# Optimization experiments

Measured on AMD Instinct MI355X. Metric: run time of the kernel, lower is better.

The kernel has to match this reference:

```python
import jax, jax.numpy as jnp
import numpy as np

N, E, G, B, L = 24576, 98304, 512, 512, 1000
F_IN, H1, C1, C2, HID = 5, 2, 64, 128, 256


def setup_inputs() -> dict:
    key = jax.random.key(0)
    ks = jax.random.split(key, 20)
    rn = lambda k, s: jax.random.normal(k, s, jnp.float32) * 0.1
    return {
        "x": jax.random.normal(ks[0], (N, F_IN), jnp.float32),
        "edge_index": jax.random.randint(ks[1], (2, E), 0, N),
        "batch": jnp.sort(jax.random.randint(ks[2], (N,), 0, G)),
        "protein_seq": jax.random.randint(ks[3], (B, L), 0, 22),
        "W1": rn(ks[4], (F_IN, H1 * C1)), "att_src1": rn(ks[5], (H1, C1)), "att_dst1": rn(ks[6], (H1, C1)), "b1": jnp.zeros((H1 * C1,), jnp.float32),
        "W2": rn(ks[7], (H1 * C1, C2)), "att_src2": rn(ks[8], (1, C2)), "att_dst2": rn(ks[9], (1, C2)), "b2": jnp.zeros((C2,), jnp.float32),
        "Wd": rn(ks[10], (C2, HID)), "bd": jnp.zeros((HID,), jnp.float32),
        "Pe": rn(ks[11], (22, 64)),
        "K1": rn(ks[12], (64, 64, 3)), "bk1": jnp.zeros((64,), jnp.float32),
        "K2": rn(ks[13], (128, 64, 5)), "bk2": jnp.zeros((128,), jnp.float32),
        "Wp": rn(ks[14], (128, HID)), "bp": jnp.zeros((HID,), jnp.float32),
        "Wf1": rn(ks[15], (2 * HID, 128)), "bf1": jnp.zeros((128,), jnp.float32),
        "Wf2": rn(ks[16], (128, 64)), "bf2": jnp.zeros((64,), jnp.float32),
        "Wo": rn(ks[17], (64, 1)), "bo": jnp.zeros((1,), jnp.float32),
    }


def _gat(x, edge_index, W, att_src, att_dst, b, heads, out_ch):
    """PyG GATConv: add self-loops, per-edge LeakyReLU(0.2) scores, segment softmax over dst."""
    n = x.shape[0]
    h = (x @ W).reshape(n, heads, out_ch)
    loop = jnp.arange(n)
    src = jnp.concatenate([edge_index[0], loop])
    dst = jnp.concatenate([edge_index[1], loop])
    a_s = jnp.sum(h * att_src[None], axis=-1)  # [n, H]
    a_d = jnp.sum(h * att_dst[None], axis=-1)
    e = jax.nn.leaky_relu(a_s[src] + a_d[dst], negative_slope=0.2)  # [E+n, H]
    m = jax.ops.segment_max(e, dst, num_segments=n)
    w = jnp.exp(e - m[dst])
    den = jax.ops.segment_sum(w, dst, num_segments=n)
    alpha = w / (den[dst] + 1e-16)
    out = jax.ops.segment_sum(h[src] * alpha[..., None], dst, num_segments=n)
    return out.reshape(n, heads * out_ch) + b


def _conv1d(x, k, pad):  # x: [B,C,L], k: [O,I,K]
    return jax.lax.conv_general_dilated(x, k, (1,), [(pad, pad)], dimension_numbers=("NCH", "OIH", "NCH"))


def reference(x, edge_index, batch, protein_seq, W1, att_src1, att_dst1, b1, W2, att_src2, att_dst2, b2, Wd, bd, Pe, K1, bk1, K2, bk2, Wp, bp, Wf1, bf1, Wf2, bf2, Wo, bo):
    # drug branch (GAT x2 + global mean pool)
    g = jax.nn.elu(_gat(x, edge_index, W1, att_src1, att_dst1, b1, H1, C1))
    g = jax.nn.elu(_gat(g, edge_index, W2, att_src2, att_dst2, b2, 1, C2))
    sums = jax.ops.segment_sum(g, batch, num_segments=G)
    cnt = jax.ops.segment_sum(jnp.ones((g.shape[0], 1), g.dtype), batch, num_segments=G)
    drug = jax.nn.relu(sums / jnp.maximum(cnt, 1.0) @ Wd + bd)
    # protein branch (embed -> conv1d x2 -> global max pool)
    pe = Pe[protein_seq].transpose(0, 2, 1)  # [B, 64, L]
    p = jax.nn.elu(_conv1d(pe, K1, 1) + bk1[None, :, None])
    p = jax.nn.elu(_conv1d(p, K2, 2) + bk2[None, :, None])
    prot = jax.nn.relu(jnp.max(p, axis=2) @ Wp + bp)
    # head
    h = jnp.concatenate([drug, prot], axis=1)
    h = jax.nn.relu(h @ Wf1 + bf1)
    h = jax.nn.relu(h @ Wf2 + bf2)
    return h @ Wo + bo
```

## Files before the change

kernel.cpp:

```cpp
#include <hip/hip_runtime.h>
#include <hip/hip_bf16.h>
#include <math.h>

#define NN 24576
#define NE 98304
#define ETOT (NE + NN)
#define NG 512
#define NB 512
#define LL 1000
#define TL 60
#define NTILE 17
#define PROT_BLKS (NB * NTILE)
#define CNT_BLKS (ETOT / 256)
#define AS1_BLKS (NN * 2 / 256)

typedef __attribute__((ext_vector_type(8))) short short8;
typedef __attribute__((ext_vector_type(4))) short short4v;
typedef __attribute__((ext_vector_type(4))) float f32x4;

__device__ inline short f2bf(float x) {
    union { __hip_bfloat16 b; short s; } u;
    u.b = __float2bfloat16(x);
    return u.s;
}

__device__ inline float bf2f(short s) {
    return __uint_as_float(((unsigned)(unsigned short)s) << 16);
}

__device__ inline void atomicMaxFloat(float* addr, float val) {
    int* ai = (int*)addr;
    int old = __float_as_int(*addr);
    while (__int_as_float(old) < val) {
        int assumed = old;
        old = atomicCAS(ai, assumed, __float_as_int(val));
        if (old == assumed) break;
    }
}

__global__ void k_init_prep(int* deg, int* cursor, float* sums, float* cnt, float* pmax,
                            const float* K1, const float* K2, const float* W2, const float* Pe,
                            const float* W1, const float* as1c, const float* ad1c,
                            const float* as2c, const float* ad2c,
                            short* Bswz2, short* Bh2, short* Bl2, float* M1,
                            float* wvec) {
    int bid = blockIdx.x, t = threadIdx.x;
    if (bid < 256) {
        int i = bid * 256 + t;
        if (i < NN) { deg[i] = 0; cursor[i] = 0; }
        if (i < NG * 128) sums[i] = 0.f;
        if (i < NG) cnt[i] = 0.f;
        if (i < NB * 128) pmax[i] = -1e30f;
        return;
    }
    int idx = (bid - 256) * 256 + t;
    if (idx < 20) {
        int q = idx % 10, hd = q / 5, f = q % 5;
        const float* av = (idx < 10) ? as1c : ad1c;
        float s = 0.f;
        for (int c = 0; c < 64; c++) s += W1[f * 128 + hd * 64 + c] * av[hd * 64 + c];
        wvec[idx < 10 ? q : 10 + q] = s;
    }
    if (idx >= 32 && idx < 288) {
        int q = idx - 32;
        int kk = q & 127;
        const float* av = (q < 128) ? as2c : ad2c;
        float s = 0.f;
        for (int n2 = 0; n2 < 128; n2++) s += W2[kk * 128 + n2] * av[n2];
        wvec[idx] = s;
    }
    if (idx < 22 * 3 * 64) {
        int tok = idx / 192, r2 = idx % 192;
        int k = r2 >> 6, oc = r2 & 63;
        float s = 0.f;
        for (int ic = 0; ic < 64; ic++) s += K1[oc * 192 + ic * 3 + k] * Pe[tok * 64 + ic];
        M1[idx] = s;
    }
    if (idx < 320 * 128) {
        int j = idx & 7, lane = (idx >> 3) & 63, rest = idx >> 9;
        int nt = rest & 7, kb = rest >> 3;
        int k = kb * 32 + ((lane >> 4) << 3) + j;
        int n = nt * 16 + (lane & 15);
        int kk = k / 64, i = k % 64;
        Bswz2[idx] = f2bf(K2[n * 320 + i * 5 + kk]);
    }
    if (idx < 128 * 128) {
        int j = idx & 7, lane = (idx >> 3) & 63, rest = idx >> 9;
        int nt = rest & 7, kb = rest >> 3;
        int k = kb * 32 + ((lane >> 4) << 3) + j;
        int n = nt * 16 + (lane & 15);
        float v = W2[k * 128 + n];
        short hh = f2bf(v);
        Bh2[idx] = hh;
        Bl2[idx] = f2bf(v - bf2f(hh));
    }
}

#define SSTR 72
__global__ __launch_bounds__(256, 6) void k_prot_cnt_as1(
    const int* seq, const float* M1, const float* bk1,
    const short* Bswz2, const float* bk2, float* pmax,
    const int* ei, int* deg,
    const float* x, const float* wvec, float* as1o, float* ad1o) {
    int bid = blockIdx.x;
    int t = threadIdx.x;

    if (bid >= PROT_BLKS) {
        int rb = bid - PROT_BLKS;
        if (rb < CNT_BLKS) {
            int e = rb * 256 + t;
            int d = (e < NE) ? ei[NE + e] : e - NE;
            atomicAdd(&deg[d], 1);
        } else {
            int idx = (rb - CNT_BLKS) * 256 + t;
            int n = idx >> 1, hd = idx & 1;
            float s = 0.f, dv = 0.f;
#pragma unroll
            for (int f = 0; f < 5; f++) {
                float xv = x[n * 5 + f];
                s += xv * wvec[hd * 5 + f];
                dv += xv * wvec[10 + hd * 5 + f];
            }
            as1o[idx] = s;
            ad1o[idx] = dv;
        }
        return;
    }

    __shared__ __align__(16) short s1[68 * SSTR];
    __shared__ int stok[68];

    int b = bid / NTILE;
    int tile = bid - b * NTILE;
    int t0 = tile * TL;

    if (t < 66) {
        int l = t0 - 3 + t;
        stok[t] = (l >= 0 && l < LL) ? seq[b * LL + l] : -1;
    }
    if (t < 36) {
        *(short8*)&s1[64 * SSTR + t * 8] = (short8){0, 0, 0, 0, 0, 0, 0, 0};
    }
    __syncthreads();

    {
        int q = t >> 2, c0 = (t & 3) << 4;
        int l = t0 - 2 + q;
        short tmp[16];
        if (l >= 0 && l < LL) {
            float v[16];
#pragma unroll
            for (int j = 0; j < 4; j++) {
                float4 bv = *(const float4*)&bk1[c0 + j * 4];
                v[j * 4 + 0] = bv.x; v[j * 4 + 1] = bv.y; v[j * 4 + 2] = bv.z; v[j * 4 + 3] = bv.w;
            }
#pragma unroll
            for (int k = 0; k < 3; k++) {
                int tok = stok[q + k];
                if (tok >= 0) {
                    const float4* mr = (const float4*)&M1[tok * 192 + k * 64 + c0];
#pragma unroll
                    for (int j = 0; j < 4; j++) {
                        float4 mv = mr[j];
                        v[j * 4 + 0] += mv.x; v[j * 4 + 1] += mv.y;
                        v[j * 4 + 2] += mv.z; v[j * 4 + 3] += mv.w;
                    }
                }
            }
#pragma unroll
            for (int j = 0; j < 16; j++) {
                float xv = v[j];
                xv = xv > 0.f ? xv : __expf(xv) - 1.f;
                tmp[j] = f2bf(xv);
            }
        } else {
#pragma unroll
            for (int j = 0; j < 16; j++) tmp[j] = 0;
        }
        *(short8*)&s1[q * SSTR + c0] = *(short8*)&tmp[0];
        *(short8*)&s1[q * SSTR + c0 + 8] = *(short8*)&tmp[8];
    }
    __syncthreads();

    int wv = t >> 6, lane = t & 63;
    int ln15 = lane & 15, quad = lane >> 4;

    f32x4 acc2[4][2];
#pragma unroll
    for (int mi = 0; mi < 4; mi++)
#pragma unroll
        for (int ni = 0; ni < 2; ni++) acc2[mi][ni] = (f32x4){0.f, 0.f, 0.f, 0.f};
#pragma unroll 2
    for (int kb = 0; kb < 10; kb++) {
        int koff = kb * 32 + quad * 8;
        int kk = koff >> 6, i0 = koff & 63;
        short8 a[4], bb[2];
#pragma unroll
        for (int mi = 0; mi < 4; mi++)
            a[mi] = *(const short8*)&s1[(mi * 16 + ln15 + kk) * SSTR + i0];
#pragma unroll
        for (int ni = 0; ni < 2; ni++)
            bb[ni] = *(const short8*)&Bswz2[((kb * 8 + wv * 2 + ni) * 64 + lane) * 8];
#pragma unroll
        for (int mi = 0; mi < 4; mi++)
#pragma unroll
            for (int ni = 0; ni < 2; ni++)
                acc2[mi][ni] = __builtin_amdgcn_mfma_f32_16x16x32_bf16(a[mi], bb[ni], acc2[mi][ni], 0, 0, 0);
    }

#pragma unroll
    for (int ni = 0; ni < 2; ni++) {
        int col = (wv * 2 + ni) * 16 + ln15;
        float mx = -1e30f;
#pragma unroll
        for (int mi = 0; mi < 4; mi++) {
#pragma unroll
            for (int r = 0; r < 4; r++) {
                int p = mi * 16 + quad * 4 + r;
                if (p < TL && t0 + p < LL) mx = fmaxf(mx, acc2[mi][ni][r]);
            }
        }
        mx = fmaxf(mx, __shfl_xor(mx, 16, 64));
        mx = fmaxf(mx, __shfl_xor(mx, 32, 64));
        if (quad == 0) {
            float v = mx + bk2[col];
            v = v > 0.f ? v : __expf(v) - 1.f;
            atomicMaxFloat(&pmax[b * 128 + col], v);
        }
    }
}

__global__ void k_scan1(const int* deg, int* excl, int* part) {
    __shared__ int s[256];
    int b = blockIdx.x, t = threadIdx.x, i = b * 256 + t;
    int v = deg[i];
    s[t] = v;
    __syncthreads();
    for (int o = 1; o < 256; o <<= 1) {
        int x = (t >= o) ? s[t - o] : 0;
        __syncthreads();
        s[t] += x;
        __syncthreads();
    }
    excl[i] = s[t] - v;
    if (t == 255) part[b] = s[t];
}

__global__ void k_scan23(const int* excl, const int* part, int* rowptr) {
    __shared__ int sp[96];
    __shared__ int pref;
    int b = blockIdx.x, t = threadIdx.x;
    if (t < 96) sp[t] = part[t];
    __syncthreads();
    if (t == 0) {
        int run = 0;
        for (int i = 0; i < b; i++) run += sp[i];
        pref = run;
    }
    __syncthreads();
    int i = b * 256 + t;
    rowptr[i] = excl[i] + pref;
    if (i == 0) rowptr[NN] = ETOT;
}

__global__ void k_scatter(const int* ei, const int* rowptr, int* cursor, int* colidx) {
    int e = blockIdx.x * 256 + threadIdx.x;
    if (e >= ETOT) return;
    int s, d;
    if (e < NE) { s = ei[e]; d = ei[NE + e]; }
    else { s = d = e - NE; }
    int pos = atomicAdd(&cursor[d], 1);
    colidx[rowptr[d] + pos] = s;
}

__global__ void k_agg2x(const int* rowptr, const int* colidx, const float* x,
                        const float* as_, const float* ad_,
                        const float* W1, const float* b1, const float* wvec,
                        unsigned int* g1b, float* as2, float* ad2) {
    __shared__ float sW[640];
    __shared__ float sb1[128];
    __shared__ float swa[256];
    int t = threadIdx.x;
    for (int i = t; i < 640; i += 256) sW[i] = W1[i];
    if (t < 128) { sb1[t] = b1[t]; swa[t] = wvec[32 + t]; swa[128 + t] = wvec[160 + t]; }
    __syncthreads();

    int d = blockIdx.x * 16 + (t >> 4);
    int g = t & 15;
    int hd = (g < 5) ? 0 : 1;
    int f = (g < 5) ? g : g - 5;
    float adv = ad_[d * 2 + hd];
    int p0 = rowptr[d], p1 = rowptr[d + 1];
    float den = 0.f, acc = 0.f;
    if (g < 10) {
        for (int pc = p0; pc < p1; pc += 4) {
            int sarr[4]; float ev[4], xv[4];
#pragma unroll
            for (int i = 0; i < 4; i++) {
                int pp = pc + i;
                sarr[i] = colidx[pp < p1 ? pp : p1 - 1];
            }
#pragma unroll
            for (int i = 0; i < 4; i++) {
                ev[i] = as_[sarr[i] * 2 + hd];
                xv[i] = x[sarr[i] * 5 + f];
            }
#pragma unroll
            for (int i = 0; i < 4; i++) {
                if (pc + i < p1) {
                    float e = ev[i] + adv;
                    e = e >= 0.f ? e : 0.2f * e;
                    float w = __expf(e);
                    den += w;
                    acc += w * xv[i];
                }
            }
        }
    }
    float xn = acc / (den + 1e-16f);
    int gb = (t & 63) & ~15;
    int hcol = g >> 3;
    float xs[5];
#pragma unroll
    for (int f2 = 0; f2 < 5; f2++)
        xs[f2] = __shfl(xn, gb + hcol * 5 + f2, 64);
    float ps = 0.f, pd = 0.f;
    float g1v[8];
#pragma unroll
    for (int k = 0; k < 8; k++) {
        int col = g * 8 + k;
        float v = sb1[col];
#pragma unroll
        for (int f2 = 0; f2 < 5; f2++) v += xs[f2] * sW[f2 * 128 + col];
        v = v > 0.f ? v : __expf(v) - 1.f;
        g1v[k] = v;
        ps += v * swa[col];
        pd += v * swa[128 + col];
    }
    uint4 pk;
    pk.x = ((unsigned)(unsigned short)f2bf(g1v[1]) << 16) | (unsigned)(unsigned short)f2bf(g1v[0]);
    pk.y = ((unsigned)(unsigned short)f2bf(g1v[3]) << 16) | (unsigned)(unsigned short)f2bf(g1v[2]);
    pk.z = ((unsigned)(unsigned short)f2bf(g1v[5]) << 16) | (unsigned)(unsigned short)f2bf(g1v[4]);
    pk.w = ((unsigned)(unsigned short)f2bf(g1v[7]) << 16) | (unsigned)(unsigned short)f2bf(g1v[6]);
    *(uint4*)&g1b[d * 64 + g * 4] = pk;
#pragma unroll
    for (int msk = 1; msk < 16; msk <<= 1) {
        ps += __shfl_xor(ps, msk, 64);
        pd += __shfl_xor(pd, msk, 64);
    }
    if (g == 0) { as2[d] = ps; ad2[d] = pd; }
}

__global__ void k_agg1y(const int* rowptr, const int* colidx, const unsigned int* hb,
                        const float* as_, const float* ad_, float* yacc) {
    int t = threadIdx.x;
    int d = blockIdx.x * 4 + (t >> 6);
    int c = t & 63;
    float adv = ad_[d];
    int p0 = rowptr[d], p1 = rowptr[d + 1];
    float den = 0.f, acc0 = 0.f, acc1 = 0.f;
    for (int pc = p0; pc < p1; pc += 4) {
        int sarr[4]; float ev[4]; unsigned int hv[4];
#pragma unroll
        for (int i = 0; i < 4; i++) {
            int pp = pc + i;
            sarr[i] = colidx[pp < p1 ? pp : p1 - 1];
        }
#pragma unroll
        for (int i = 0; i < 4; i++) {
            ev[i] = as_[sarr[i]];
            hv[i] = hb[sarr[i] * 64 + c];
        }
#pragma unroll
        for (int i = 0; i < 4; i++) {
            if (pc + i < p1) {
                float e = ev[i] + adv;
                e = e >= 0.f ? e : 0.2f * e;
                float w = __expf(e);
                den += w;
                acc0 += w * __uint_as_float(hv[i] << 16);
                acc1 += w * __uint_as_float(hv[i] & 0xFFFF0000u);
            }
        }
    }
    float inv = 1.f / (den + 1e-16f);
    ((float2*)yacc)[d * 64 + c] = (float2){acc0 * inv, acc1 * inv};
}

#define ASTR 136
__global__ __launch_bounds__(256, 2) void k_g2mm(
    const float* yacc, const short* Bh, const short* Bl, const float* b2, float* g2) {
    __shared__ __align__(16) short Ah[64 * ASTR];
    __shared__ __align__(16) short Al[64 * ASTR];
    int t = threadIdx.x;
    int m0 = blockIdx.x * 64;
    int wv = t >> 6, lane = t & 63;
    int ln15 = lane & 15, quad = lane >> 4;

    for (int i = t; i < 64 * 32; i += 256) {
        int row = i >> 5, c4 = (i & 31) * 4;
        float4 v = *(const float4*)&yacc[(m0 + row) * 128 + c4];
        short4v hi, lo;
        hi.x = f2bf(v.x); lo.x = f2bf(v.x - bf2f(hi.x));
        hi.y = f2bf(v.y); lo.y = f2bf(v.y - bf2f(hi.y));
        hi.z = f2bf(v.z); lo.z = f2bf(v.z - bf2f(hi.z));
        hi.w = f2bf(v.w); lo.w = f2bf(v.w - bf2f(hi.w));
        *(short4v*)&Ah[row * ASTR + c4] = hi;
        *(short4v*)&Al[row * ASTR + c4] = lo;
    }
    __syncthreads();

    f32x4 acc[8];
#pragma unroll
    for (int nt = 0; nt < 8; nt++) acc[nt] = (f32x4){0.f, 0.f, 0.f, 0.f};
    int arow = wv * 16 + ln15;
#pragma unroll
    for (int kb = 0; kb < 4; kb++) {
        int koff = kb * 32 + quad * 8;
        short8 a_hi = *(const short8*)&Ah[arow * ASTR + koff];
        short8 a_lo = *(const short8*)&Al[arow * ASTR + koff];
#pragma unroll
        for (int nt = 0; nt < 8; nt++) {
            short8 bh = *(const short8*)&Bh[((kb * 8 + nt) * 64 + lane) * 8];
            short8 bl = *(const short8*)&Bl[((kb * 8 + nt) * 64 + lane) * 8];
            acc[nt] = __builtin_amdgcn_mfma_f32_16x16x32_bf16(a_hi, bh, acc[nt], 0, 0, 0);
            acc[nt] = __builtin_amdgcn_mfma_f32_16x16x32_bf16(a_hi, bl, acc[nt], 0, 0, 0);
            acc[nt] = __builtin_amdgcn_mfma_f32_16x16x32_bf16(a_lo, bh, acc[nt], 0, 0, 0);
        }
    }
#pragma unroll
    for (int nt = 0; nt < 8; nt++) {
        int col = nt * 16 + ln15;
        float bias = b2[col];
#pragma unroll
        for (int r = 0; r < 4; r++) {
            float v = acc[nt][r] + bias;
            v = v > 0.f ? v : __expf(v) - 1.f;
            int n = m0 + wv * 16 + quad * 4 + r;
            g2[n * 128 + col] = v;
        }
    }
}

__global__ void k_pool(const float* g2, const int* batch, float* sums, float* cnt) {
    __shared__ int sb[96];
    int blk = blockIdx.x, j = threadIdx.x;
    int n0 = blk * 96;
    if (j < 96) sb[j] = batch[n0 + j];
    __syncthreads();
    float v[4];
#pragma unroll
    for (int i = 0; i < 4; i++) v[i] = g2[(n0 + i) * 128 + j];
    int cur = sb[0], runStart = 0;
    float acc = 0.f;
    for (int q0 = 0; q0 < 96; q0 += 4) {
        float nv[4] = {0.f, 0.f, 0.f, 0.f};
        if (q0 + 4 < 96) {
#pragma unroll
            for (int i = 0; i < 4; i++) nv[i] = g2[(n0 + q0 + 4 + i) * 128 + j];
        }
#pragma unroll
        for (int i = 0; i < 4; i++) {
            int q = q0 + i;
            int bb = sb[q];
            if (bb != cur) {
                atomicAdd(&sums[cur * 128 + j], acc);
                if (j == 0) atomicAdd(&cnt[cur], (float)(q - runStart));
                cur = bb; acc = 0.f; runStart = q;
            }
            acc += v[i];
        }
#pragma unroll
        for (int i = 0; i < 4; i++) v[i] = nv[i];
    }
    atomicAdd(&sums[cur * 128 + j], acc);
    if (j == 0) atomicAdd(&cnt[cur], (float)(96 - runStart));
}

__global__ __launch_bounds__(512) void k_tail(
    const float* pmax, const float* Wp, const float* bp,
    const float* sums, const float* cnt, const float* Wd, const float* bd,
    const float* Wf1, const float* bf1, const float* Wf2, const float* bf2,
    const float* Wo, const float* bo, float* out) {
    __shared__ float in2[512];
    __shared__ float part1[512];
    __shared__ float hh[128];
    __shared__ float part2[512];
    __shared__ float h2s[64];
    int g = blockIdx.x, t = threadIdx.x;

    if (t < 256) {
        float pacc = bp[t];
#pragma unroll 8
        for (int i = 0; i < 128; i++) pacc += pmax[g * 128 + i] * Wp[i * 256 + t];
        in2[256 + t] = pacc > 0.f ? pacc : 0.f;
    } else {
        int o = t - 256;
        float c = cnt[g]; c = c < 1.f ? 1.f : c;
        float inv = 1.f / c;
        float dacc = bd[o];
#pragma unroll 8
        for (int i = 0; i < 128; i++) dacc += sums[g * 128 + i] * inv * Wd[i * 256 + o];
        in2[o] = dacc > 0.f ? dacc : 0.f;
    }
    __syncthreads();

    {
        int o = t >> 2, ks = t & 3;
        float p = 0.f;
        int c0 = ks * 128;
#pragma unroll 8
        for (int cc = c0; cc < c0 + 128; cc++) p += in2[cc] * Wf1[cc * 128 + o];
        part1[t] = p;
    }
    __syncthreads();
    if (t < 128) {
        float a = bf1[t] + part1[t * 4] + part1[t * 4 + 1] + part1[t * 4 + 2] + part1[t * 4 + 3];
        hh[t] = a > 0.f ? a : 0.f;
    }
    __syncthreads();

    {
        int o = t >> 3, ks = t & 7;
        float p = 0.f;
        int c0 = ks * 16;
#pragma unroll
        for (int cc = c0; cc < c0 + 16; cc++) p += hh[cc] * Wf2[cc * 64 + o];
        part2[t] = p;
    }
    __syncthreads();
    if (t < 64) {
        float a = bf2[t];
#pragma unroll
        for (int k = 0; k < 8; k++) a += part2[t * 8 + k];
        h2s[t] = a > 0.f ? a : 0.f;
    }
    __syncthreads();

    if (t < 64) {
        float p = h2s[t] * Wo[t];
#pragma unroll
        for (int off = 32; off > 0; off >>= 1) p += __shfl_down(p, off, 64);
        if (t == 0) out[g] = p + bo[0];
    }
}

extern "C" void kernel_launch(void* const* d_in, const int* in_sizes, int n_in,
                              void* d_out, int out_size, void* d_ws, size_t ws_size,
                              hipStream_t stream) {
    (void)in_sizes; (void)n_in; (void)out_size; (void)ws_size;
    const float* x   = (const float*)d_in[0];
    const int* ei    = (const int*)d_in[1];
    const int* batch = (const int*)d_in[2];
    const int* seq   = (const int*)d_in[3];
    const float* W1  = (const float*)d_in[4];
    const float* a_s1 = (const float*)d_in[5];
    const float* a_d1 = (const float*)d_in[6];
    const float* b1  = (const float*)d_in[7];
    const float* W2  = (const float*)d_in[8];
    const float* a_s2 = (const float*)d_in[9];
    const float* a_d2 = (const float*)d_in[10];
    const float* b2  = (const float*)d_in[11];
    const float* Wd  = (const float*)d_in[12];
    const float* bd  = (const float*)d_in[13];
    const float* Pe  = (const float*)d_in[14];
    const float* K1  = (const float*)d_in[15];
    const float* bk1 = (const float*)d_in[16];
    const float* K2  = (const float*)d_in[17];
    const float* bk2 = (const float*)d_in[18];
    const float* Wp  = (const float*)d_in[19];
    const float* bp  = (const float*)d_in[20];
    const float* Wf1 = (const float*)d_in[21];
    const float* bf1 = (const float*)d_in[22];
    const float* Wf2 = (const float*)d_in[23];
    const float* bf2 = (const float*)d_in[24];
    const float* Wo  = (const float*)d_in[25];
    const float* bo  = (const float*)d_in[26];
    float* out = (float*)d_out;

    float* w = (float*)d_ws;
    float* g1bf = w; w += NN * 64;
    float* yacc = w; w += NN * 128;
    float* g2   = w; w += NN * 128;
    float* as1  = w; w += NN * 2;
    float* ad1  = w; w += NN * 2;
    float* as2  = w; w += NN;
    float* ad2  = w; w += NN;
    float* sums = w; w += NG * 128;
    float* cnt  = w; w += NG;
    float* pmax = w; w += NB * 128;
    float* wvec = w; w += 512;
    short* Bswz2 = (short*)w; w += 320 * 128 / 2;
    short* Bh2  = (short*)w; w += 128 * 128 / 2;
    short* Bl2  = (short*)w; w += 128 * 128 / 2;
    float* M1   = w; w += 22 * 3 * 64;
    int* deg    = (int*)w; w += NN;
    int* cursor = (int*)w; w += NN;
    int* excl   = (int*)w; w += NN;
    int* part   = (int*)w; w += 128;
    int* rowptr = (int*)w; w += NN + 8;
    int* colidx = (int*)w; w += ETOT;

    unsigned int* g1b = (unsigned int*)g1bf;

    hipLaunchKernelGGL(k_init_prep, dim3(256 + 160), dim3(256), 0, stream,
                       deg, cursor, sums, cnt, pmax,
                       K1, K2, W2, Pe, W1, a_s1, a_d1, a_s2, a_d2,
                       Bswz2, Bh2, Bl2, M1, wvec);

    hipLaunchKernelGGL(k_prot_cnt_as1, dim3(PROT_BLKS + CNT_BLKS + AS1_BLKS), dim3(256), 0, stream,
                       seq, M1, bk1, Bswz2, bk2, pmax,
                       ei, deg, x, wvec, as1, ad1);

    hipLaunchKernelGGL(k_scan1, dim3(NN / 256), dim3(256), 0, stream, deg, excl, part);
    hipLaunchKernelGGL(k_scan23, dim3(NN / 256), dim3(256), 0, stream, excl, part, rowptr);
    hipLaunchKernelGGL(k_scatter, dim3(ETOT / 256), dim3(256), 0, stream, ei, rowptr, cursor, colidx);

    hipLaunchKernelGGL(k_agg2x, dim3(NN / 16), dim3(256), 0, stream,
                       rowptr, colidx, x, as1, ad1, W1, b1, wvec, g1b, as2, ad2);

    hipLaunchKernelGGL(k_agg1y, dim3(NN / 4), dim3(256), 0, stream,
                       rowptr, colidx, g1b, as2, ad2, yacc);

    hipLaunchKernelGGL(k_g2mm, dim3(NN / 64), dim3(256), 0, stream,
                       yacc, Bh2, Bl2, b2, g2);

    hipLaunchKernelGGL(k_pool, dim3(NN / 96), dim3(128), 0, stream, g2, batch, sums, cnt);

    hipLaunchKernelGGL(k_tail, dim3(NG), dim3(512), 0, stream,
                       pmax, Wp, bp, sums, cnt, Wd, bd, Wf1, bf1, Wf2, bf2, Wo, bo, out);
}
```

Before: 294.9 us.

## Replace pmax atomics with per-tile partials and pack node records for gathers

The protein conv kernel now writes a per-tile partial max to a buffer instead of doing CAS-loop atomic max. The bias, ELU and reduction over the tiles move into the tail kernel, which also drops the pmax init. Node features x and the layer-1 attention scalars are packed into one 16-float record per node, so each gather in k_agg2x hits a single 64-byte record. The token staging in shared memory and its barrier are removed, and tokens are read straight from global memory. This trades atomic contention and scattered gathers for a larger partial buffer and redundant token loads.

```diff
diff --git a/kernel.cpp b/kernel.cpp
--- a/kernel.cpp
+++ b/kernel.cpp
@@ -28,17 +28,7 @@
     return __uint_as_float(((unsigned)(unsigned short)s) << 16);
 }
 
-__device__ inline void atomicMaxFloat(float* addr, float val) {
-    int* ai = (int*)addr;
-    int old = __float_as_int(*addr);
-    while (__int_as_float(old) < val) {
-        int assumed = old;
-        old = atomicCAS(ai, assumed, __float_as_int(val));
-        if (old == assumed) break;
-    }
-}
-
-__global__ void k_init_prep(int* deg, int* cursor, float* sums, float* cnt, float* pmax,
+__global__ void k_init_prep(int* deg, int* cursor, float* sums, float* cnt,
                             const float* K1, const float* K2, const float* W2, const float* Pe,
                             const float* W1, const float* as1c, const float* ad1c,
                             const float* as2c, const float* ad2c,
@@ -50,7 +40,6 @@
         if (i < NN) { deg[i] = 0; cursor[i] = 0; }
         if (i < NG * 128) sums[i] = 0.f;
         if (i < NG) cnt[i] = 0.f;
-        if (i < NB * 128) pmax[i] = -1e30f;
         return;
     }
     int idx = (bid - 256) * 256 + t;
@@ -99,9 +88,9 @@
 #define SSTR 72
 __global__ __launch_bounds__(256, 6) void k_prot_cnt_as1(
     const int* seq, const float* M1, const float* bk1,
-    const short* Bswz2, const float* bk2, float* pmax,
+    const short* Bswz2, float* pmaxp,
     const int* ei, int* deg,
-    const float* x, const float* wvec, float* as1o, float* ad1o) {
+    const float* x, const float* wvec, float* rec) {
     int bid = blockIdx.x;
     int t = threadIdx.x;
 
@@ -114,34 +103,35 @@
         } else {
             int idx = (rb - CNT_BLKS) * 256 + t;
             int n = idx >> 1, hd = idx & 1;
+            float xv[5];
             float s = 0.f, dv = 0.f;
 #pragma unroll
             for (int f = 0; f < 5; f++) {
-                float xv = x[n * 5 + f];
-                s += xv * wvec[hd * 5 + f];
-                dv += xv * wvec[10 + hd * 5 + f];
-            }
-            as1o[idx] = s;
-            ad1o[idx] = dv;
+                xv[f] = x[n * 5 + f];
+                s += xv[f] * wvec[hd * 5 + f];
+                dv += xv[f] * wvec[10 + hd * 5 + f];
+            }
+            float* rr = &rec[n * 16];
+            if (hd == 0) {
+#pragma unroll
+                for (int f = 0; f < 5; f++) rr[f] = xv[f];
+                rr[5] = s; rr[7] = dv;
+            } else {
+                rr[6] = s; rr[8] = dv;
+            }
         }
         return;
     }
 
     __shared__ __align__(16) short s1[68 * SSTR];
-    __shared__ int stok[68];
 
     int b = bid / NTILE;
     int tile = bid - b * NTILE;
     int t0 = tile * TL;
 
-    if (t < 66) {
-        int l = t0 - 3 + t;
-        stok[t] = (l >= 0 && l < LL) ? seq[b * LL + l] : -1;
-    }
     if (t < 36) {
         *(short8*)&s1[64 * SSTR + t * 8] = (short8){0, 0, 0, 0, 0, 0, 0, 0};
     }
-    __syncthreads();
 
     {
         int q = t >> 2, c0 = (t & 3) << 4;
@@ -156,8 +146,9 @@
             }
 #pragma unroll
             for (int k = 0; k < 3; k++) {
-                int tok = stok[q + k];
-                if (tok >= 0) {
+                int lp = l - 1 + k;
+                if (lp >= 0 && lp < LL) {
+                    int tok = seq[b * LL + lp];
                     const float4* mr = (const float4*)&M1[tok * 192 + k * 64 + c0];
 #pragma unroll
                     for (int j = 0; j < 4; j++) {
@@ -222,11 +213,7 @@
         }
         mx = fmaxf(mx, __shfl_xor(mx, 16, 64));
         mx = fmaxf(mx, __shfl_xor(mx, 32, 64));
-        if (quad == 0) {
-            float v = mx + bk2[col];
-            v = v > 0.f ? v : __expf(v) - 1.f;
-            atomicMaxFloat(&pmax[b * 128 + col], v);
-        }
+        if (quad == 0) pmaxp[(b * NTILE + tile) * 128 + col] = mx;
     }
 }
 
@@ -273,8 +260,7 @@
     colidx[rowptr[d] + pos] = s;
 }
 
-__global__ void k_agg2x(const int* rowptr, const int* colidx, const float* x,
-                        const float* as_, const float* ad_,
+__global__ void k_agg2x(const int* rowptr, const int* colidx, const float* rec,
                         const float* W1, const float* b1, const float* wvec,
                         unsigned int* g1b, float* as2, float* ad2) {
     __shared__ float sW[640];
@@ -289,7 +275,7 @@
     int g = t & 15;
     int hd = (g < 5) ? 0 : 1;
     int f = (g < 5) ? g : g - 5;
-    float adv = ad_[d * 2 + hd];
+    float adv = rec[d * 16 + 7 + hd];
     int p0 = rowptr[d], p1 = rowptr[d + 1];
     float den = 0.f, acc = 0.f;
     if (g < 10) {
@@ -302,8 +288,8 @@
             }
 #pragma unroll
             for (int i = 0; i < 4; i++) {
-                ev[i] = as_[sarr[i] * 2 + hd];
-                xv[i] = x[sarr[i] * 5 + f];
+                ev[i] = rec[sarr[i] * 16 + 5 + hd];
+                xv[i] = rec[sarr[i] * 16 + f];
             }
 #pragma unroll
             for (int i = 0; i < 4; i++) {
@@ -478,10 +464,11 @@
 }
 
 __global__ __launch_bounds__(512) void k_tail(
-    const float* pmax, const float* Wp, const float* bp,
+    const float* pmaxp, const float* bk2, const float* Wp, const float* bp,
     const float* sums, const float* cnt, const float* Wd, const float* bd,
     const float* Wf1, const float* bf1, const float* Wf2, const float* bf2,
     const float* Wo, const float* bo, float* out) {
+    __shared__ float spm[128];
     __shared__ float in2[512];
     __shared__ float part1[512];
     __shared__ float hh[128];
@@ -489,10 +476,20 @@
     __shared__ float h2s[64];
     int g = blockIdx.x, t = threadIdx.x;
 
+    if (t < 128) {
+        float m = -1e30f;
+#pragma unroll
+        for (int tt = 0; tt < NTILE; tt++)
+            m = fmaxf(m, pmaxp[(g * NTILE + tt) * 128 + t]);
+        float v = m + bk2[t];
+        spm[t] = v > 0.f ? v : __expf(v) - 1.f;
+    }
+    __syncthreads();
+
     if (t < 256) {
         float pacc = bp[t];
 #pragma unroll 8
-        for (int i = 0; i < 128; i++) pacc += pmax[g * 128 + i] * Wp[i * 256 + t];
+        for (int i = 0; i < 128; i++) pacc += spm[i] * Wp[i * 256 + t];
         in2[256 + t] = pacc > 0.f ? pacc : 0.f;
     } else {
         int o = t - 256;
@@ -582,13 +579,12 @@
     float* g1bf = w; w += NN * 64;
     float* yacc = w; w += NN * 128;
     float* g2   = w; w += NN * 128;
-    float* as1  = w; w += NN * 2;
-    float* ad1  = w; w += NN * 2;
     float* as2  = w; w += NN;
     float* ad2  = w; w += NN;
     float* sums = w; w += NG * 128;
     float* cnt  = w; w += NG;
-    float* pmax = w; w += NB * 128;
+    float* pmaxp = w; w += NB * NTILE * 128;
+    float* rec  = w; w += NN * 16;
     float* wvec = w; w += 512;
     short* Bswz2 = (short*)w; w += 320 * 128 / 2;
     short* Bh2  = (short*)w; w += 128 * 128 / 2;
@@ -604,20 +600,20 @@
     unsigned int* g1b = (unsigned int*)g1bf;
 
     hipLaunchKernelGGL(k_init_prep, dim3(256 + 160), dim3(256), 0, stream,
-                       deg, cursor, sums, cnt, pmax,
+                       deg, cursor, sums, cnt,
                        K1, K2, W2, Pe, W1, a_s1, a_d1, a_s2, a_d2,
                        Bswz2, Bh2, Bl2, M1, wvec);
 
     hipLaunchKernelGGL(k_prot_cnt_as1, dim3(PROT_BLKS + CNT_BLKS + AS1_BLKS), dim3(256), 0, stream,
-                       seq, M1, bk1, Bswz2, bk2, pmax,
-                       ei, deg, x, wvec, as1, ad1);
+                       seq, M1, bk1, Bswz2, pmaxp,
+                       ei, deg, x, wvec, rec);
 
     hipLaunchKernelGGL(k_scan1, dim3(NN / 256), dim3(256), 0, stream, deg, excl, part);
     hipLaunchKernelGGL(k_scan23, dim3(NN / 256), dim3(256), 0, stream, excl, part, rowptr);
     hipLaunchKernelGGL(k_scatter, dim3(ETOT / 256), dim3(256), 0, stream, ei, rowptr, cursor, colidx);
 
     hipLaunchKernelGGL(k_agg2x, dim3(NN / 16), dim3(256), 0, stream,
-                       rowptr, colidx, x, as1, ad1, W1, b1, wvec, g1b, as2, ad2);
+                       rowptr, colidx, rec, W1, b1, wvec, g1b, as2, ad2);
 
     hipLaunchKernelGGL(k_agg1y, dim3(NN / 4), dim3(256), 0, stream,
                        rowptr, colidx, g1b, as2, ad2, yacc);
@@ -628,5 +624,5 @@
     hipLaunchKernelGGL(k_pool, dim3(NN / 96), dim3(128), 0, stream, g2, batch, sums, cnt);
 
     hipLaunchKernelGGL(k_tail, dim3(NG), dim3(512), 0, stream,
-                       pmax, Wp, bp, sums, cnt, Wd, bd, Wf1, bf1, Wf2, bf2, Wo, bo, out);
-}
+                       pmaxp, bk2, Wp, bp, sums, cnt, Wd, bd, Wf1, bf1, Wf2, bf2, Wo, bo, out);
+}
```

After: 271.4 us. -8.0%, faster.
